# Optimization experiments

Hardware: AMD Instinct MI355X
Metric: run time of the kernel (lower is better)

Reference implementation:

```python
import jax, jax.numpy as jnp
import numpy as np

B, S, D = 1, 2048, 2048
H, HKV = 16, 4
HD = D // H  # 128
E, TOPK, F = 8, 2, 2048
CLIP = 8.0
THETA = 500000.0
EPS = 1e-5


def setup_inputs() -> dict:
    key = jax.random.key(0)
    ks = jax.random.split(key, 12)
    s = lambda k, shape, scale: jax.random.normal(k, shape, dtype=jnp.float32) * scale
    return {
        "hidden_states": s(ks[0], (B, S, D), 1.0),
        "position_ids": jnp.broadcast_to(jnp.arange(S, dtype=jnp.int32), (B, S)),
        "ln1_w": jnp.ones((D,), jnp.float32),
        "ln1_b": jnp.zeros((D,), jnp.float32),
        "ln2_w": jnp.ones((D,), jnp.float32),
        "ln2_b": jnp.zeros((D,), jnp.float32),
        "Wqkv": s(ks[1], (D, (H + 2 * HKV) * HD), 0.02),
        "Wout": s(ks[2], (D, D), 0.02),
        "Wrouter": s(ks[3], (D, E), 0.02),
        "w1": s(ks[4], (E, D, F), 0.02),
        "v1": s(ks[5], (E, D, F), 0.02),
        "w2": s(ks[6], (E, F, D), 0.02),
    }


def _layernorm(x, w, b):
    mu = jnp.mean(x, axis=-1, keepdims=True)
    var = jnp.mean((x - mu) ** 2, axis=-1, keepdims=True)
    return (x - mu) * jax.lax.rsqrt(var + EPS) * w + b


def _rope(x, pos):
    # x: [B,S,h,HD], neox style (rotate halves)
    half = HD // 2
    inv_freq = 1.0 / (THETA ** (jnp.arange(0, HD, 2, dtype=jnp.float32) / HD))
    ang = pos.astype(jnp.float32)[..., None] * inv_freq  # [B,S,half]
    cos = jnp.cos(ang)[:, :, None, :]
    sin = jnp.sin(ang)[:, :, None, :]
    x1, x2 = x[..., :half], x[..., half:]
    return jnp.concatenate([x1 * cos - x2 * sin, x2 * cos + x1 * sin], axis=-1)


def _forward(hidden_states, position_ids, ln1_w, ln1_b, ln2_w, ln2_b,
             Wqkv, Wout, Wrouter, w1, v1, w2):
    residual = hidden_states
    h = _layernorm(hidden_states, ln1_w, ln1_b)
    qkv = jnp.clip(h @ Wqkv, -CLIP, CLIP)
    q, k, v = jnp.split(qkv, [H * HD, H * HD + HKV * HD], axis=-1)
    q = q.reshape(B, S, H, HD)
    k = k.reshape(B, S, HKV, HD)
    v = v.reshape(B, S, HKV, HD)
    q = _rope(q, position_ids)
    k = _rope(k, position_ids)
    # GQA: repeat kv heads
    rep = H // HKV
    k = jnp.repeat(k, rep, axis=2)
    v = jnp.repeat(v, rep, axis=2)
    scale = HD ** -0.5
    scores = jnp.einsum("bqhd,bkhd->bhqk", q, k) * scale
    causal = jnp.tril(jnp.ones((S, S), dtype=bool))
    scores = jnp.where(causal, scores, jnp.float32(-1e9))
    probs = jax.nn.softmax(scores, axis=-1)
    attn = jnp.einsum("bhqk,bkhd->bqhd", probs, v).reshape(B, S, D)
    attn = attn @ Wout
    h = residual + attn
    residual = h
    h = _layernorm(h, ln2_w, ln2_b)

    # MoE over flattened tokens
    x = h.reshape(-1, D)  # [T,D]
    logits = x @ Wrouter  # [T,E]
    rw = jax.nn.softmax(logits.astype(jnp.float32), axis=-1)
    top_w, top_idx = jax.lax.top_k(rw, TOPK)  # [T,TOPK]
    top_w = top_w / jnp.sum(top_w, axis=-1, keepdims=True)
    acc = jnp.zeros_like(x)
    for e in range(E):  # fixed small expert count, matches source structure
        ew = jnp.sum(top_w * (top_idx == e), axis=-1, keepdims=True)  # [T,1]
        inter = jax.nn.silu(x @ w1[e]) * (x @ v1[e])
        acc = acc + (inter @ w2[e]) * ew
    out = acc.reshape(B, S, D) + residual
    return out


def reference(hidden_states, position_ids, ln1_w, ln1_b, ln2_w, ln2_b,
              Wqkv, Wout, Wrouter, w1, v1, w2):
    return _forward(hidden_states, position_ids, ln1_w, ln1_b, ln2_w, ln2_b,
                    Wqkv, Wout, Wrouter, w1, v1, w2)
```

## Files before the change

kernel.cpp:

```cpp
#include <hip/hip_runtime.h>
#include <cstdint>
#include <cstddef>
#include <cmath>

typedef unsigned short u16;
typedef unsigned int u32;
typedef __attribute__((ext_vector_type(8))) _Float16 f16x8;
typedef __attribute__((ext_vector_type(4))) float f32x4;

#define S_LEN 2048
#define DMODEL 2048
#define NHEAD 16
#define NKVH 4
#define HDIM 128
#define NQKV 3072
#define NF 2048
#define TA 4096
#define ATT_SCALE 0.08838834764831845f
#define LO_SCALE 1024.0f
#define LO_INV (1.0f/1024.0f)
#define DEFER_THR 8.0f

static __device__ __forceinline__ u16 f2h(float x){ _Float16 h=(_Float16)x; return __builtin_bit_cast(u16,h); }
static __device__ __forceinline__ float h2f(u16 u){ return (float)__builtin_bit_cast(_Float16,u); }
static __device__ __forceinline__ void split2(float x, u16& hi, u16& lo){
  hi = f2h(x);
  lo = f2h((x - h2f(hi)) * LO_SCALE);
}
static __device__ __forceinline__ void gload16(const u16* g, u16* l){
  __builtin_amdgcn_global_load_lds(
      (const __attribute__((address_space(1))) void*)g,
      (__attribute__((address_space(3))) void*)l, 16, 0, 0);
}
static __device__ __forceinline__ void xcd_swz(int& bx, int& by){
  int gx = gridDim.x;
  int n = gx * gridDim.y;
  int bid = by*gx + bx;
  int cpx = n >> 3;
  int s = (bid & 7)*cpx + (bid >> 3);
  bx = s % gx; by = s / gx;
}

#define WS_WOUTH ((size_t)0)
#define WS_WOUTL ((size_t)8388608)
#define WS_QKVTH ((size_t)16777216)
#define WS_QKVTL ((size_t)29360128)
#define WS_H1H   ((size_t)41943040)
#define WS_H1L   ((size_t)50331648)
#define WS_QKV   ((size_t)58720256)
#define WS_QH    ((size_t)16777216)
#define WS_QL    ((size_t)25165824)
#define WS_KH    ((size_t)33554432)
#define WS_KL    ((size_t)35651584)
#define WS_VTH   ((size_t)37748736)
#define WS_VTL   ((size_t)39845888)
#define WS_OH    ((size_t)41943040)
#define WS_OL    ((size_t)50331648)
#define WS_H2    ((size_t)58720256)
#define WS_X2    ((size_t)75497472)
#define WS_I1    ((size_t)0)
#define WS_Y     ((size_t)16777216)
#define WS_MOE   ((size_t)33554432)
#define WS_SM    ((size_t)83886080)
#define WS_WT0   ((size_t)84934656)
#define WS_WT1   ((size_t)152043520)
#define WS_BIG   ((size_t)219152384)
#define SM_INVT   0
#define SM_COUNTS 256
#define SM_FILL   320
#define SM_OFFS   384
#define SM_NT     448
#define SM_TE     512
#define SM_TRS    768
#define SM_E01    1024
#define SM_W01    (1024+16384)
#define SM_ATOK   (1024+2*16384)
#define SM_AW     (1024+3*16384)
#define SM_SLOT   (1024+4*16384)

__global__ void __launch_bounds__(64) init_k(int* counts, int* fill, float* invt){
  int t = threadIdx.x;
  if (t < 8) { counts[t] = 0; fill[t] = 0; }
  double di = (double)t * (1.0/64.0);
  float y = (float)pow(500000.0, di);
  invt[t] = 1.0f / y;
}

__global__ void __launch_bounds__(256) wsplit_k(const float* __restrict__ W,
    u16* __restrict__ Th, u16* __restrict__ Tl, int N){
  __shared__ float tile[32][33];
  int n0 = blockIdx.x*32, k0 = blockIdx.y*32;
  int tid = threadIdx.x;
  int rr = tid >> 3, cg = tid & 7;
  #pragma unroll
  for (int j=0;j<4;++j)
    tile[rr][cg*4+j] = W[(size_t)(k0+rr)*N + n0 + cg*4 + j];
  __syncthreads();
  int cc = tid >> 3, sg = tid & 7;
  #pragma unroll
  for (int j=0;j<4;++j){
    float x = tile[sg*4+j][cc];
    u16 hi, lo; split2(x, hi, lo);
    size_t idx = (size_t)(n0+cc)*2048 + k0 + sg*4 + j;
    Th[idx] = hi; Tl[idx] = lo;
  }
}

__global__ void __launch_bounds__(256) wconvT_k(const float* __restrict__ W,
                                                u16* __restrict__ T){
  __shared__ float tile[64][68];
  int n0 = blockIdx.x*64, k0 = blockIdx.y*64;
  size_t ebase = (size_t)blockIdx.z * 2048 * 2048;
  int tid = threadIdx.x;
  int rr = tid >> 4, c4 = (tid & 15)*4;
  #pragma unroll
  for (int p=0;p<4;++p){
    float4 v = *(const float4*)(W + ebase + (size_t)(k0+p*16+rr)*2048 + n0 + c4);
    *(float4*)&tile[p*16+rr][c4] = v;
  }
  __syncthreads();
  int nn = tid >> 2, kc = (tid & 3)*16;
  u16 buf[16];
  #pragma unroll
  for (int j=0;j<16;++j) buf[j] = f2h(tile[kc+j][nn]);
  u16* dst = T + ebase + (size_t)(n0+nn)*2048 + k0 + kc;
  *(int4*)dst = *(int4*)&buf[0];
  *(int4*)(dst+8) = *(int4*)&buf[8];
}

__device__ __forceinline__ float blk_red_sum(float v, float* red, int tid){
  #pragma unroll
  for (int off=1; off<64; off<<=1) v += __shfl_xor(v, off);
  if ((tid&63)==0) red[tid>>6] = v;
  __syncthreads();
  float r = red[0]+red[1]+red[2]+red[3];
  __syncthreads();
  return r;
}

__global__ void __launch_bounds__(256) ln1_k(const float* __restrict__ X,
    const float* __restrict__ W, const float* __restrict__ Bv,
    u16* __restrict__ Hh, u16* __restrict__ Hl){
  __shared__ float red[4];
  int t = blockIdx.x, tid = threadIdx.x;
  const float* row = X + (size_t)t*DMODEL + tid*8;
  float4 a = *(const float4*)row;
  float4 b = *(const float4*)(row+4);
  float xs[8] = {a.x,a.y,a.z,a.w,b.x,b.y,b.z,b.w};
  float s = 0.f;
  #pragma unroll
  for (int j=0;j<8;++j) s += xs[j];
  float mu = blk_red_sum(s, red, tid) * (1.f/DMODEL);
  float sq = 0.f;
  #pragma unroll
  for (int j=0;j<8;++j){ float d = xs[j]-mu; sq += d*d; }
  float var = blk_red_sum(sq, red, tid) * (1.f/DMODEL);
  float rs = 1.0f/sqrtf(var + 1e-5f);
  float4 w0 = *(const float4*)(W + tid*8);
  float4 w1 = *(const float4*)(W + tid*8 + 4);
  float4 b0 = *(const float4*)(Bv + tid*8);
  float4 b1 = *(const float4*)(Bv + tid*8 + 4);
  float ws_[8] = {w0.x,w0.y,w0.z,w0.w,w1.x,w1.y,w1.z,w1.w};
  float bs_[8] = {b0.x,b0.y,b0.z,b0.w,b1.x,b1.y,b1.z,b1.w};
  u32 ph[4], pl[4];
  #pragma unroll
  for (int j=0;j<4;++j){
    u16 h0,l0,h1,l1;
    split2((xs[2*j]-mu)*rs*ws_[2*j]+bs_[2*j], h0, l0);
    split2((xs[2*j+1]-mu)*rs*ws_[2*j+1]+bs_[2*j+1], h1, l1);
    ph[j] = (u32)h0 | ((u32)h1<<16);
    pl[j] = (u32)l0 | ((u32)l1<<16);
  }
  int4 vh; vh.x=(int)ph[0]; vh.y=(int)ph[1]; vh.z=(int)ph[2]; vh.w=(int)ph[3];
  int4 vl; vl.x=(int)pl[0]; vl.y=(int)pl[1]; vl.z=(int)pl[2]; vl.w=(int)pl[3];
  *(int4*)(Hh + (size_t)t*DMODEL + tid*8) = vh;
  *(int4*)(Hl + (size_t)t*DMODEL + tid*8) = vl;
}

template<int MODE>
__global__ void __launch_bounds__(256) gemm32_k(
    const u16* __restrict__ Ahp, const u16* __restrict__ Alp,
    const u16* __restrict__ Bhp, const u16* __restrict__ Blp,
    float* __restrict__ C, const float* __restrict__ res)
{
  constexpr int K = 2048;
  __shared__ u16 Ash[128*32], Asl[128*32], Bsh[64*32], Bsl[64*32];
  int bx = blockIdx.x, by = blockIdx.y;
  xcd_swz(bx, by);
  int m0 = by*128, n0 = bx*64;
  int tid = threadIdx.x, w = tid>>6, lane = tid&63;
  int l15 = lane&15, l4 = lane>>4, wr = w>>1, wc = w&1;
  int srow = lane>>2;
  int scol = ((lane&3) ^ ((lane>>3)&3))*8;

  f32x4 accH[4][2] = {}, accC[4][2] = {};

  for (int k0 = 0; k0 < K; k0 += 32){
    __syncthreads();
    #pragma unroll
    for (int c=0;c<2;++c){
      int row = w*32 + c*16 + srow;
      size_t ga = (size_t)(m0+row)*K + k0 + scol;
      gload16(Ahp+ga, &Ash[(w*32+c*16)*32]);
      gload16(Alp+ga, &Asl[(w*32+c*16)*32]);
    }
    {
      int rowb = w*16 + srow;
      size_t gb = (size_t)(n0+rowb)*K + k0 + scol;
      gload16(Bhp+gb, &Bsh[(w*16)*32]);
      gload16(Blp+gb, &Bsl[(w*16)*32]);
    }
    __syncthreads();
    int fsl = (l4 ^ ((l15>>1)&3))*8;
    f16x8 ah[4], al[4];
    #pragma unroll
    for (int mi=0; mi<4; ++mi){
      int row = wr*64 + mi*16 + l15;
      ah[mi] = *(const f16x8*)&Ash[row*32 + fsl];
      al[mi] = *(const f16x8*)&Asl[row*32 + fsl];
    }
    #pragma unroll
    for (int ni=0; ni<2; ++ni){
      int row = wc*32 + ni*16 + l15;
      f16x8 bh = *(const f16x8*)&Bsh[row*32 + fsl];
      f16x8 bl = *(const f16x8*)&Bsl[row*32 + fsl];
      #pragma unroll
      for (int mi=0; mi<4; ++mi){
        accH[mi][ni] = __builtin_amdgcn_mfma_f32_16x16x32_f16(ah[mi], bh, accH[mi][ni], 0,0,0);
        accC[mi][ni] = __builtin_amdgcn_mfma_f32_16x16x32_f16(ah[mi], bl, accC[mi][ni], 0,0,0);
        accC[mi][ni] = __builtin_amdgcn_mfma_f32_16x16x32_f16(al[mi], bh, accC[mi][ni], 0,0,0);
      }
    }
  }

  #pragma unroll
  for (int mi=0; mi<4; ++mi){
    #pragma unroll
    for (int ni=0; ni<2; ++ni){
      #pragma unroll
      for (int r=0; r<4; ++r){
        int rl = wr*64 + mi*16 + l4*4 + r;
        int cl = wc*32 + ni*16 + l15;
        float v = accH[mi][ni][r] + accC[mi][ni][r]*LO_INV;
        if constexpr (MODE == 0){
          v = fminf(fmaxf(v, -8.f), 8.f);
          C[(size_t)(m0 + rl)*NQKV + n0 + cl] = v;
        } else {
          size_t idx = (size_t)(m0 + rl)*DMODEL + n0 + cl;
          C[idx] = v + res[idx];
        }
      }
    }
  }
}

__global__ void __launch_bounds__(256) rope_k(const float* __restrict__ qkv,
    const int* __restrict__ pos_ids, const float* __restrict__ invt,
    u16* __restrict__ Qh, u16* __restrict__ Ql, u16* __restrict__ Kh, u16* __restrict__ Kl){
  int s = blockIdx.x;
  float pos = (float)pos_ids[s];
  const float* row = qkv + (size_t)s*NQKV;
  for (int p = threadIdx.x; p < 1280; p += 256){
    int i = p & 63;
    float ang = pos * invt[i];
    float sn, cs;
    sincosf(ang, &sn, &cs);
    u16 h1_,l1_,h2_,l2_;
    if (p < 1024){
      int h = p >> 6;
      float x1 = row[h*HDIM + i];
      float x2 = row[h*HDIM + 64 + i];
      size_t base = ((size_t)h*S_LEN + s)*HDIM;
      split2(x1*cs - x2*sn, h1_, l1_);
      split2(x2*cs + x1*sn, h2_, l2_);
      Qh[base + i] = h1_; Ql[base + i] = l1_;
      Qh[base + 64 + i] = h2_; Ql[base + 64 + i] = l2_;
    } else {
      int kh = (p-1024) >> 6;
      float x1 = row[2048 + kh*HDIM + i];
      float x2 = row[2048 + kh*HDIM + 64 + i];
      size_t base = ((size_t)kh*S_LEN + s)*HDIM;
      split2(x1*cs - x2*sn, h1_, l1_);
      split2(x2*cs + x1*sn, h2_, l2_);
      Kh[base + i] = h1_; Kl[base + i] = l1_;
      Kh[base + 64 + i] = h2_; Kl[base + 64 + i] = l2_;
    }
  }
}

__global__ void __launch_bounds__(256) vtrans_k(const float* __restrict__ qkv,
    u16* __restrict__ Vth, u16* __restrict__ Vtl){
  __shared__ float tile[32][33];
  int s0 = blockIdx.x*32, c0 = blockIdx.y*32;
  int tid = threadIdx.x;
  int rr = tid >> 3, cg = tid & 7;
  #pragma unroll
  for (int j=0;j<4;++j)
    tile[rr][cg*4+j] = qkv[(size_t)(s0+rr)*NQKV + 2560 + c0 + cg*4 + j];
  __syncthreads();
  int cc = tid >> 3, sg = tid & 7;
  #pragma unroll
  for (int j=0;j<4;++j){
    float x = tile[sg*4+j][cc];
    u16 hi, lo; split2(x, hi, lo);
    size_t idx = (size_t)(c0+cc)*S_LEN + s0 + sg*4 + j;
    Vth[idx] = hi; Vtl[idx] = lo;
  }
}

__global__ void __launch_bounds__(256) attn_k(
    const u16* __restrict__ Qhp, const u16* __restrict__ Qlp,
    const u16* __restrict__ Khp, const u16* __restrict__ Klp,
    const u16* __restrict__ Vthp, const u16* __restrict__ Vtlp,
    u16* __restrict__ Oh, u16* __restrict__ Ol){
  __shared__ u16 Ksh[32*128], Ksl[32*128];
  __shared__ u16 Vsh[128*32], Vsl[128*32];
  __shared__ u16 Psh[4*16*40], Psl[4*16*40];
  int tid = threadIdx.x;
  int w = tid>>6, lane = tid&63, l15 = lane&15, l4 = lane>>4;
  int qb = 31 - blockIdx.x;
  int h = blockIdx.y, kvh = h>>2;
  int q0 = qb*64 + w*16;
  f16x8 qfh[4], qfl[4];
  #pragma unroll
  for (int ds=0; ds<4; ++ds){
    size_t off = ((size_t)h*S_LEN + q0 + l15)*HDIM + ds*32 + l4*8;
    qfh[ds] = *(const f16x8*)(Qhp + off);
    qfl[ds] = *(const f16x8*)(Qlp + off);
  }
  f32x4 accH[8] = {}, accC[8] = {};
  float m_r[4], l_r[4];
  #pragma unroll
  for (int r=0;r<4;++r){ m_r[r] = -1e30f; l_r[r] = 0.f; }
  int ntile = 2*qb + 2;
  for (int kb = 0; kb < ntile; ++kb){
    int kbase = kb*32;
    __syncthreads();
    #pragma unroll
    for (int c=0;c<2;++c){
      int krow = w*8 + c*4 + (lane>>4);
      int ks = lane&15;
      int kcol = ((ks&8) | ((ks&7) ^ (krow&7)))*8;
      size_t koff = ((size_t)kvh*S_LEN + kbase + krow)*HDIM + kcol;
      gload16(Khp + koff, &Ksh[(w*8+c*4)*128]);
      gload16(Klp + koff, &Ksl[(w*8+c*4)*128]);
      int vrow = w*32 + c*16 + (lane>>2);
      int vcol = (((lane&3) ^ ((lane>>3)&3)))*8;
      size_t voff = ((size_t)kvh*HDIM + vrow)*S_LEN + kbase + vcol;
      gload16(Vthp + voff, &Vsh[(w*32+c*16)*32]);
      gload16(Vtlp + voff, &Vsl[(w*32+c*16)*32]);
    }
    __syncthreads();
    f32x4 sH0 = {}, sH1 = {}, sC0 = {}, sC1 = {};
    #pragma unroll
    for (int ds=0; ds<4; ++ds){
      int ksl = ds*4 + l4;
      int klds = ((ksl&8) | ((ksl&7) ^ (l15&7)))*8;
      f16x8 kh0 = *(const f16x8*)&Ksh[l15*128 + klds];
      f16x8 kl0 = *(const f16x8*)&Ksl[l15*128 + klds];
      f16x8 kh1 = *(const f16x8*)&Ksh[(16+l15)*128 + klds];
      f16x8 kl1 = *(const f16x8*)&Ksl[(16+l15)*128 + klds];
      sH0 = __builtin_amdgcn_mfma_f32_16x16x32_f16(qfh[ds], kh0, sH0, 0,0,0);
      sC0 = __builtin_amdgcn_mfma_f32_16x16x32_f16(qfh[ds], kl0, sC0, 0,0,0);
      sC0 = __builtin_amdgcn_mfma_f32_16x16x32_f16(qfl[ds], kh0, sC0, 0,0,0);
      sH1 = __builtin_amdgcn_mfma_f32_16x16x32_f16(qfh[ds], kh1, sH1, 0,0,0);
      sC1 = __builtin_amdgcn_mfma_f32_16x16x32_f16(qfh[ds], kl1, sC1, 0,0,0);
      sC1 = __builtin_amdgcn_mfma_f32_16x16x32_f16(qfl[ds], kh1, sC1, 0,0,0);
    }
    float v0[4], v1[4];
    bool need = false;
    #pragma unroll
    for (int r=0;r<4;++r){
      int qg = q0 + l4*4 + r;
      v0[r] = (sH0[r] + sC0[r]*LO_INV)*ATT_SCALE; if (kbase + l15 > qg) v0[r] = -1e9f;
      v1[r] = (sH1[r] + sC1[r]*LO_INV)*ATT_SCALE; if (kbase + 16 + l15 > qg) v1[r] = -1e9f;
      float pm = fmaxf(v0[r], v1[r]);
      need = need || (pm > m_r[r] + DEFER_THR);
    }
    if (__any(need)){
      float fac[4];
      #pragma unroll
      for (int r=0;r<4;++r){
        float mx = fmaxf(v0[r], v1[r]);
        mx = fmaxf(mx, __shfl_xor(mx,1));
        mx = fmaxf(mx, __shfl_xor(mx,2));
        mx = fmaxf(mx, __shfl_xor(mx,4));
        mx = fmaxf(mx, __shfl_xor(mx,8));
        float mnew = fmaxf(m_r[r], mx);
        fac[r] = __expf(m_r[r] - mnew);
        l_r[r] *= fac[r];
        m_r[r] = mnew;
      }
      #pragma unroll
      for (int nt=0; nt<8; ++nt){
        #pragma unroll
        for (int r=0;r<4;++r){ accH[nt][r] *= fac[r]; accC[nt][r] *= fac[r]; }
      }
    }
    #pragma unroll
    for (int r=0;r<4;++r){
      float p0 = __expf(v0[r] - m_r[r]);
      float p1 = __expf(v1[r] - m_r[r]);
      l_r[r] += p0 + p1;
      u16 hi, lo;
      split2(p0, hi, lo);
      Psh[w*640 + (l4*4+r)*40 + l15] = hi;
      Psl[w*640 + (l4*4+r)*40 + l15] = lo;
      split2(p1, hi, lo);
      Psh[w*640 + (l4*4+r)*40 + 16 + l15] = hi;
      Psl[w*640 + (l4*4+r)*40 + 16 + l15] = lo;
    }
    f16x8 pfh = *(const f16x8*)&Psh[w*640 + l15*40 + l4*8];
    f16x8 pfl = *(const f16x8*)&Psl[w*640 + l15*40 + l4*8];
    #pragma unroll
    for (int nt=0; nt<8; ++nt){
      int vsl = (l4 ^ ((l15>>1)&3))*8;
      f16x8 vh = *(const f16x8*)&Vsh[(nt*16 + l15)*32 + vsl];
      f16x8 vl = *(const f16x8*)&Vsl[(nt*16 + l15)*32 + vsl];
      accH[nt] = __builtin_amdgcn_mfma_f32_16x16x32_f16(pfh, vh, accH[nt], 0,0,0);
      f32x4 aC = __builtin_amdgcn_mfma_f32_16x16x32_f16(pfh, vl, accC[nt], 0,0,0);
      accC[nt] = __builtin_amdgcn_mfma_f32_16x16x32_f16(pfl, vh, aC, 0,0,0);
    }
  }
  #pragma unroll
  for (int r=0;r<4;++r){
    float l = l_r[r];
    l += __shfl_xor(l,1); l += __shfl_xor(l,2);
    l += __shfl_xor(l,4); l += __shfl_xor(l,8);
    l_r[r] = l;
  }
  #pragma unroll
  for (int nt=0; nt<8; ++nt){
    #pragma unroll
    for (int r=0;r<4;++r){
      int row = q0 + l4*4 + r;
      int col = h*HDIM + nt*16 + l15;
      float val = (accH[nt][r] + accC[nt][r]*LO_INV) / l_r[r];
      u16 hi, lo; split2(val, hi, lo);
      Oh[(size_t)row*DMODEL + col] = hi;
      Ol[(size_t)row*DMODEL + col] = lo;
    }
  }
}

__global__ void __launch_bounds__(256) ln2_router_k(const float* __restrict__ H2,
    const float* __restrict__ W, const float* __restrict__ Bv,
    const float* __restrict__ Wr, u16* __restrict__ X2,
    int* __restrict__ e01, float* __restrict__ w01, int* __restrict__ counts){
  __shared__ float red[4];
  __shared__ float lred[4][8];
  int t = blockIdx.x, tid = threadIdx.x;
  const float* row = H2 + (size_t)t*DMODEL + tid*8;
  float4 a = *(const float4*)row;
  float4 b = *(const float4*)(row+4);
  float xs[8] = {a.x,a.y,a.z,a.w,b.x,b.y,b.z,b.w};
  float s = 0.f;
  #pragma unroll
  for (int j=0;j<8;++j) s += xs[j];
  float mu = blk_red_sum(s, red, tid) * (1.f/DMODEL);
  float sq = 0.f;
  #pragma unroll
  for (int j=0;j<8;++j){ float d = xs[j]-mu; sq += d*d; }
  float var = blk_red_sum(sq, red, tid) * (1.f/DMODEL);
  float rs = 1.0f/sqrtf(var + 1e-5f);
  float4 w0 = *(const float4*)(W + tid*8);
  float4 w1 = *(const float4*)(W + tid*8 + 4);
  float4 b0 = *(const float4*)(Bv + tid*8);
  float4 b1 = *(const float4*)(Bv + tid*8 + 4);
  float ws_[8] = {w0.x,w0.y,w0.z,w0.w,w1.x,w1.y,w1.z,w1.w};
  float bs_[8] = {b0.x,b0.y,b0.z,b0.w,b1.x,b1.y,b1.z,b1.w};
  float xn[8];
  #pragma unroll
  for (int j=0;j<8;++j) xn[j] = (xs[j]-mu)*rs*ws_[j]+bs_[j];
  u32 pk[4];
  #pragma unroll
  for (int j=0;j<4;++j) pk[j] = (u32)f2h(xn[2*j]) | ((u32)f2h(xn[2*j+1])<<16);
  int4 v; v.x=(int)pk[0]; v.y=(int)pk[1]; v.z=(int)pk[2]; v.w=(int)pk[3];
  *(int4*)(X2 + (size_t)t*DMODEL + tid*8) = v;
  float lg[8] = {0,0,0,0,0,0,0,0};
  #pragma unroll
  for (int j=0;j<8;++j){
    const float* wrp = Wr + (size_t)(tid*8 + j)*8;
    float4 wa = *(const float4*)wrp;
    float4 wb = *(const float4*)(wrp+4);
    lg[0]+=xn[j]*wa.x; lg[1]+=xn[j]*wa.y; lg[2]+=xn[j]*wa.z; lg[3]+=xn[j]*wa.w;
    lg[4]+=xn[j]*wb.x; lg[5]+=xn[j]*wb.y; lg[6]+=xn[j]*wb.z; lg[7]+=xn[j]*wb.w;
  }
  #pragma unroll
  for (int e=0;e<8;++e){
    #pragma unroll
    for (int off=1; off<64; off<<=1) lg[e] += __shfl_xor(lg[e], off);
  }
  if ((tid&63)==0){
    #pragma unroll
    for (int e=0;e<8;++e) lred[tid>>6][e] = lg[e];
  }
  __syncthreads();
  if (tid==0){
    float L[8];
    #pragma unroll
    for (int e=0;e<8;++e) L[e] = lred[0][e]+lred[1][e]+lred[2][e]+lred[3][e];
    int e0 = 0;
    #pragma unroll
    for (int e=1;e<8;++e) if (L[e] > L[e0]) e0 = e;
    int e1 = (e0==0)?1:0;
    #pragma unroll
    for (int e=0;e<8;++e) if (e!=e0 && L[e] > L[e1]) e1 = e;
    float ax = expf(L[e1]-L[e0]);
    float z = 1.f/(1.f+ax);
    e01[2*t] = e0; e01[2*t+1] = e1;
    w01[2*t] = z;  w01[2*t+1] = ax*z;
    atomicAdd(&counts[e0],1); atomicAdd(&counts[e1],1);
  }
}

__global__ void __launch_bounds__(64) htiles_k(const int* counts, int* offs, int* ntl,
                                               int* te, int* trs){
  if (threadIdx.x==0){
    int off=0;
    for (int e=0;e<8;++e){ offs[e]=off; off+=counts[e]; }
    offs[8]=off;
    int nt=0;
    for (int e=0;e<8;++e)
      for (int j=0; j*128 < counts[e]; ++j){ te[nt]=e; trs[nt]=j*128; nt++; }
    ntl[0]=nt;
  }
}

__global__ void __launch_bounds__(256) scatter_k(const int* __restrict__ e01,
    const float* __restrict__ w01, const int* __restrict__ offs, int* __restrict__ fill,
    int* __restrict__ atok, float* __restrict__ aw, int* __restrict__ slots){
  int t = blockIdx.x*256 + threadIdx.x;
  if (t >= S_LEN) return;
  int e0 = e01[2*t], e1 = e01[2*t+1];
  int p0 = offs[e0] + atomicAdd(&fill[e0],1);
  atok[p0] = t; aw[p0] = w01[2*t]; slots[2*t] = p0;
  int p1 = offs[e1] + atomicAdd(&fill[e1],1);
  atok[p1] = t; aw[p1] = w01[2*t+1]; slots[2*t+1] = p1;
}

__global__ void __launch_bounds__(256) gemm_moe13_k(
    const u16* __restrict__ A, const u16* __restrict__ B1T, const u16* __restrict__ B2T,
    u16* __restrict__ Y,
    const int* __restrict__ atok, const int* __restrict__ counts,
    const int* __restrict__ offs, const int* __restrict__ ntl,
    const int* __restrict__ te, const int* __restrict__ trs)
{
  constexpr int K = 2048;
  __shared__ u16 As[128*32], B1s[64*32], B2s[64*32];
  int bx = blockIdx.x, by = blockIdx.y;
  xcd_swz(bx, by);
  if (by >= ntl[0]) return;
  int e = te[by];
  int rsu = trs[by];
  int base = offs[e] + rsu;
  int valid = min(128, counts[e] - rsu);
  const u16* B1p = B1T + (size_t)e * 2048 * 2048;
  const u16* B2p = B2T + (size_t)e * 2048 * 2048;
  int tid = threadIdx.x, w = tid>>6, lane = tid&63;
  int l15 = lane & 15, l4 = lane >> 4;
  int wr = w >> 1, wc = w & 1;
  int srow = lane>>2;
  int scol = ((lane&3) ^ ((lane>>3)&3))*8;
  int n0 = bx*64;
  int tokc[2];
  #pragma unroll
  for (int c=0;c<2;++c){
    int rr = w*32 + c*16 + srow;
    tokc[c] = atok[min(base + rr, TA-1)] & (S_LEN-1);
  }

  f32x4 acc1[4][2] = {}, acc2[4][2] = {};

  for (int k0 = 0; k0 < K; k0 += 32){
    __syncthreads();
    #pragma unroll
    for (int c=0;c<2;++c)
      gload16(A + (size_t)tokc[c]*K + k0 + scol, &As[(w*32+c*16)*32]);
    {
      int rowb = w*16 + srow;
      size_t gb = (size_t)(n0+rowb)*K + k0 + scol;
      gload16(B1p + gb, &B1s[(w*16)*32]);
      gload16(B2p + gb, &B2s[(w*16)*32]);
    }
    __syncthreads();
    int fsl = (l4 ^ ((l15>>1)&3))*8;
    f16x8 af[4];
    #pragma unroll
    for (int mi=0; mi<4; ++mi)
      af[mi] = *(const f16x8*)&As[(wr*64 + mi*16 + l15)*32 + fsl];
    #pragma unroll
    for (int ni=0; ni<2; ++ni){
      int row = wc*32 + ni*16 + l15;
      f16x8 b1 = *(const f16x8*)&B1s[row*32 + fsl];
      f16x8 b2 = *(const f16x8*)&B2s[row*32 + fsl];
      #pragma unroll
      for (int mi=0; mi<4; ++mi){
        acc1[mi][ni] = __builtin_amdgcn_mfma_f32_16x16x32_f16(af[mi], b1, acc1[mi][ni], 0,0,0);
        acc2[mi][ni] = __builtin_amdgcn_mfma_f32_16x16x32_f16(af[mi], b2, acc2[mi][ni], 0,0,0);
      }
    }
  }

  #pragma unroll
  for (int mi=0; mi<4; ++mi){
    #pragma unroll
    for (int ni=0; ni<2; ++ni){
      #pragma unroll
      for (int r=0; r<4; ++r){
        int rl = wr*64 + mi*16 + l4*4 + r;
        if (rl >= valid) continue;
        int col = n0 + wc*32 + ni*16 + l15;
        float a = acc1[mi][ni][r];
        float sl = a / (1.f + __expf(-a));
        Y[(size_t)(base + rl)*NF + col] = f2h(sl * acc2[mi][ni][r]);
      }
    }
  }
}

template<int MODE>
__global__ void __launch_bounds__(256) gemm_moe_k(
    const u16* __restrict__ A, const u16* __restrict__ BT, void* __restrict__ C,
    const u16* __restrict__ i1g, const float* __restrict__ aw,
    const int* __restrict__ atok, const int* __restrict__ counts,
    const int* __restrict__ offs, const int* __restrict__ ntl,
    const int* __restrict__ te, const int* __restrict__ trs)
{
  constexpr int K = 2048;
  __shared__ u16 As[128*32], Bs[64*32];
  int bx = blockIdx.x, by = blockIdx.y;
  xcd_swz(bx, by);
  if (by >= ntl[0]) return;
  int e = te[by];
  int rsu = trs[by];
  int base = offs[e] + rsu;
  int valid = min(128, counts[e] - rsu);
  const u16* Bp = BT + (size_t)e * 2048 * 2048;
  int tid = threadIdx.x, w = tid>>6, lane = tid&63;
  int l15 = lane & 15, l4 = lane >> 4;
  int wr = w >> 1, wc = w & 1;
  int srow = lane>>2;
  int scol = ((lane&3) ^ ((lane>>3)&3))*8;
  int n0 = bx*64;
  int tokc[2];
  #pragma unroll
  for (int c=0;c<2;++c){
    int rr = w*32 + c*16 + srow;
    if constexpr (MODE == 2 || MODE == 3)
      tokc[c] = atok[min(base + rr, TA-1)] & (S_LEN-1);
    else
      tokc[c] = min(base + rr, TA-1);
  }

  f32x4 acc[4][2] = {};

  for (int k0 = 0; k0 < K; k0 += 32){
    __syncthreads();
    #pragma unroll
    for (int c=0;c<2;++c)
      gload16(A + (size_t)tokc[c]*K + k0 + scol, &As[(w*32+c*16)*32]);
    {
      int rowb = w*16 + srow;
      gload16(Bp + (size_t)(n0+rowb)*K + k0 + scol, &Bs[(w*16)*32]);
    }
    __syncthreads();
    int fsl = (l4 ^ ((l15>>1)&3))*8;
    f16x8 af[4];
    #pragma unroll
    for (int mi=0; mi<4; ++mi)
      af[mi] = *(const f16x8*)&As[(wr*64 + mi*16 + l15)*32 + fsl];
    #pragma unroll
    for (int ni=0; ni<2; ++ni){
      f16x8 bfv = *(const f16x8*)&Bs[(wc*32 + ni*16 + l15)*32 + fsl];
      #pragma unroll
      for (int mi=0; mi<4; ++mi)
        acc[mi][ni] = __builtin_amdgcn_mfma_f32_16x16x32_f16(af[mi], bfv, acc[mi][ni], 0,0,0);
    }
  }

  #pragma unroll
  for (int mi=0; mi<4; ++mi){
    #pragma unroll
    for (int ni=0; ni<2; ++ni){
      f32x4 v = acc[mi][ni];
      #pragma unroll
      for (int r=0; r<4; ++r){
        int rl = wr*64 + mi*16 + l4*4 + r;
        if (rl >= valid) continue;
        int col = n0 + wc*32 + ni*16 + l15;
        if constexpr (MODE == 2){
          ((u16*)C)[(size_t)(base + rl)*NF + col] = f2h(v[r]);
        } else if constexpr (MODE == 3){
          size_t idx = (size_t)(base + rl)*NF + col;
          float a = h2f(i1g[idx]);
          float sl = a / (1.f + __expf(-a));
          ((u16*)C)[idx] = f2h(sl * v[r]);
        } else {
          float wgt = aw[base + rl];
          ((u16*)C)[(size_t)(base + rl)*DMODEL + col] = f2h(v[r] * wgt);
        }
      }
    }
  }
}

__global__ void __launch_bounds__(256) combine_k(const float* __restrict__ H2,
    const u16* __restrict__ MOE, const int* __restrict__ slots, float* __restrict__ out){
  int t = blockIdx.x, tid = threadIdx.x;
  int s0 = slots[2*t], s1 = slots[2*t+1];
  const float* h2p = H2 + (size_t)t*DMODEL + tid*8;
  int4 b0 = *(const int4*)(MOE + (size_t)s0*DMODEL + tid*8);
  int4 b1 = *(const int4*)(MOE + (size_t)s1*DMODEL + tid*8);
  const u16* bp0 = (const u16*)&b0;
  const u16* bp1 = (const u16*)&b1;
  float* op = out + (size_t)t*DMODEL + tid*8;
  #pragma unroll
  for (int j=0;j<8;++j)
    op[j] = h2p[j] + h2f(bp0[j]) + h2f(bp1[j]);
}

extern "C" void kernel_launch(void* const* d_in, const int* in_sizes, int n_in,
                              void* d_out, int out_size, void* d_ws, size_t ws_size,
                              hipStream_t stream){
  const float* hidden = (const float*)d_in[0];
  const int*   pos    = (const int*)d_in[1];
  const float* ln1w   = (const float*)d_in[2];
  const float* ln1b   = (const float*)d_in[3];
  const float* ln2w   = (const float*)d_in[4];
  const float* ln2b   = (const float*)d_in[5];
  const float* Wqkv   = (const float*)d_in[6];
  const float* Wout   = (const float*)d_in[7];
  const float* Wr     = (const float*)d_in[8];
  const float* w1     = (const float*)d_in[9];
  const float* v1     = (const float*)d_in[10];
  const float* w2     = (const float*)d_in[11];
  float* out = (float*)d_out;
  char* ws = (char*)d_ws;

  u16* woutTh = (u16*)(ws + WS_WOUTH);
  u16* woutTl = (u16*)(ws + WS_WOUTL);
  u16* qkvTh  = (u16*)(ws + WS_QKVTH);
  u16* qkvTl  = (u16*)(ws + WS_QKVTL);
  u16* h1h = (u16*)(ws + WS_H1H);
  u16* h1l = (u16*)(ws + WS_H1L);
  float* qkv = (float*)(ws + WS_QKV);
  u16* Qh = (u16*)(ws + WS_QH);
  u16* Ql = (u16*)(ws + WS_QL);
  u16* Kh = (u16*)(ws + WS_KH);
  u16* Kl = (u16*)(ws + WS_KL);
  u16* Vth = (u16*)(ws + WS_VTH);
  u16* Vtl = (u16*)(ws + WS_VTL);
  u16* Oh = (u16*)(ws + WS_OH);
  u16* Ol = (u16*)(ws + WS_OL);
  float* h2 = (float*)(ws + WS_H2);
  u16* x2 = (u16*)(ws + WS_X2);
  u16* i1 = (u16*)(ws + WS_I1);
  u16* Yb = (u16*)(ws + WS_Y);
  u16* moe = (u16*)(ws + WS_MOE);
  u16* wT0 = (u16*)(ws + WS_WT0);
  u16* wT1 = (u16*)(ws + WS_WT1);
  char* sm = ws + WS_SM;
  float* invt = (float*)(sm + SM_INVT);
  int* counts = (int*)(sm + SM_COUNTS);
  int* fill   = (int*)(sm + SM_FILL);
  int* offs   = (int*)(sm + SM_OFFS);
  int* ntl    = (int*)(sm + SM_NT);
  int* te     = (int*)(sm + SM_TE);
  int* trs    = (int*)(sm + SM_TRS);
  int* e01    = (int*)(sm + SM_E01);
  float* w01  = (float*)(sm + SM_W01);
  int* atok   = (int*)(sm + SM_ATOK);
  float* aw   = (float*)(sm + SM_AW);
  int* slots  = (int*)(sm + SM_SLOT);

  init_k<<<1, 64, 0, stream>>>(counts, fill, invt);
  wsplit_k<<<dim3(96,64), 256, 0, stream>>>(Wqkv, qkvTh, qkvTl, NQKV);
  wsplit_k<<<dim3(64,64), 256, 0, stream>>>(Wout, woutTh, woutTl, DMODEL);
  ln1_k<<<S_LEN, 256, 0, stream>>>(hidden, ln1w, ln1b, h1h, h1l);
  gemm32_k<0><<<dim3(48,16), 256, 0, stream>>>(h1h, h1l, qkvTh, qkvTl, qkv, nullptr);
  rope_k<<<S_LEN, 256, 0, stream>>>(qkv, pos, invt, Qh, Ql, Kh, Kl);
  vtrans_k<<<dim3(64,16), 256, 0, stream>>>(qkv, Vth, Vtl);
  attn_k<<<dim3(32,16), 256, 0, stream>>>(Qh, Ql, Kh, Kl, Vth, Vtl, Oh, Ol);
  gemm32_k<1><<<dim3(32,16), 256, 0, stream>>>(Oh, Ol, woutTh, woutTl, h2, hidden);
  ln2_router_k<<<S_LEN, 256, 0, stream>>>(h2, ln2w, ln2b, Wr, x2, e01, w01, counts);
  htiles_k<<<1, 64, 0, stream>>>(counts, offs, ntl, te, trs);
  scatter_k<<<8, 256, 0, stream>>>(e01, w01, offs, fill, atok, aw, slots);
  if (ws_size >= WS_BIG){
    wconvT_k<<<dim3(32,32,8), 256, 0, stream>>>(w1, wT0);
    wconvT_k<<<dim3(32,32,8), 256, 0, stream>>>(v1, wT1);
    gemm_moe13_k<<<dim3(32,40), 256, 0, stream>>>(x2, wT0, wT1, Yb,
        atok, counts, offs, ntl, te, trs);
    wconvT_k<<<dim3(32,32,8), 256, 0, stream>>>(w2, wT0);
    gemm_moe_k<4><<<dim3(32,40), 256, 0, stream>>>(Yb, wT0, moe, nullptr, aw,
        atok, counts, offs, ntl, te, trs);
  } else {
    wconvT_k<<<dim3(32,32,8), 256, 0, stream>>>(w1, wT0);
    gemm_moe_k<2><<<dim3(32,40), 256, 0, stream>>>(x2, wT0, i1, nullptr, nullptr,
        atok, counts, offs, ntl, te, trs);
    wconvT_k<<<dim3(32,32,8), 256, 0, stream>>>(v1, wT0);
    gemm_moe_k<3><<<dim3(32,40), 256, 0, stream>>>(x2, wT0, Yb, i1, nullptr,
        atok, counts, offs, ntl, te, trs);
    wconvT_k<<<dim3(32,32,8), 256, 0, stream>>>(w2, wT0);
    gemm_moe_k<4><<<dim3(32,40), 256, 0, stream>>>(Yb, wT0, moe, nullptr, aw,
        atok, counts, offs, ntl, te, trs);
  }
  combine_k<<<S_LEN, 256, 0, stream>>>(h2, moe, slots, out);
}
```

Baseline: 791.5 us.

## Double-buffer LDS tiles in GEMM and attention kernels, tweak attention scheduling

Gives the split-precision QKV/out GEMM, both MoE GEMMs and the attention kernel two LDS buffers each. The next K tile (or KV tile) is now prefetched while the current one is consumed, which removes one barrier per iteration and overlaps global-to-LDS loads with MFMA work. Attention also raises wave priority around its MFMA blocks and applies the causal mask only on diagonal tiles. It alternates the query-block order between head halves to balance the causal workload. The cost is doubled shared-memory use per block, which may lower occupancy, most of all in attention.

```diff
diff --git a/kernel.cpp b/kernel.cpp
--- a/kernel.cpp
+++ b/kernel.cpp
@@ -184,7 +184,7 @@
     float* __restrict__ C, const float* __restrict__ res)
 {
   constexpr int K = 2048;
-  __shared__ u16 Ash[128*32], Asl[128*32], Bsh[64*32], Bsl[64*32];
+  __shared__ u16 Ash[2][128*32], Asl[2][128*32], Bsh[2][64*32], Bsl[2][64*32];
   int bx = blockIdx.x, by = blockIdx.y;
   xcd_swz(bx, by);
   int m0 = by*128, n0 = bx*64;
@@ -195,35 +195,38 @@
 
   f32x4 accH[4][2] = {}, accC[4][2] = {};
 
-  for (int k0 = 0; k0 < K; k0 += 32){
-    __syncthreads();
+  auto stage = [&](int k0, int b){
     #pragma unroll
     for (int c=0;c<2;++c){
       int row = w*32 + c*16 + srow;
       size_t ga = (size_t)(m0+row)*K + k0 + scol;
-      gload16(Ahp+ga, &Ash[(w*32+c*16)*32]);
-      gload16(Alp+ga, &Asl[(w*32+c*16)*32]);
-    }
-    {
-      int rowb = w*16 + srow;
-      size_t gb = (size_t)(n0+rowb)*K + k0 + scol;
-      gload16(Bhp+gb, &Bsh[(w*16)*32]);
-      gload16(Blp+gb, &Bsl[(w*16)*32]);
-    }
+      gload16(Ahp+ga, &Ash[b][(w*32+c*16)*32]);
+      gload16(Alp+ga, &Asl[b][(w*32+c*16)*32]);
+    }
+    int rowb = w*16 + srow;
+    size_t gb = (size_t)(n0+rowb)*K + k0 + scol;
+    gload16(Bhp+gb, &Bsh[b][(w*16)*32]);
+    gload16(Blp+gb, &Bsl[b][(w*16)*32]);
+  };
+
+  stage(0, 0);
+  int cur = 0;
+  for (int k0 = 0; k0 < K; k0 += 32){
     __syncthreads();
+    if (k0 + 32 < K) stage(k0 + 32, cur^1);
     int fsl = (l4 ^ ((l15>>1)&3))*8;
     f16x8 ah[4], al[4];
     #pragma unroll
     for (int mi=0; mi<4; ++mi){
       int row = wr*64 + mi*16 + l15;
-      ah[mi] = *(const f16x8*)&Ash[row*32 + fsl];
-      al[mi] = *(const f16x8*)&Asl[row*32 + fsl];
+      ah[mi] = *(const f16x8*)&Ash[cur][row*32 + fsl];
+      al[mi] = *(const f16x8*)&Asl[cur][row*32 + fsl];
     }
     #pragma unroll
     for (int ni=0; ni<2; ++ni){
       int row = wc*32 + ni*16 + l15;
-      f16x8 bh = *(const f16x8*)&Bsh[row*32 + fsl];
-      f16x8 bl = *(const f16x8*)&Bsl[row*32 + fsl];
+      f16x8 bh = *(const f16x8*)&Bsh[cur][row*32 + fsl];
+      f16x8 bl = *(const f16x8*)&Bsl[cur][row*32 + fsl];
       #pragma unroll
       for (int mi=0; mi<4; ++mi){
         accH[mi][ni] = __builtin_amdgcn_mfma_f32_16x16x32_f16(ah[mi], bh, accH[mi][ni], 0,0,0);
@@ -231,6 +234,7 @@
         accC[mi][ni] = __builtin_amdgcn_mfma_f32_16x16x32_f16(al[mi], bh, accC[mi][ni], 0,0,0);
       }
     }
+    cur ^= 1;
   }
 
   #pragma unroll
@@ -313,13 +317,13 @@
     const u16* __restrict__ Khp, const u16* __restrict__ Klp,
     const u16* __restrict__ Vthp, const u16* __restrict__ Vtlp,
     u16* __restrict__ Oh, u16* __restrict__ Ol){
-  __shared__ u16 Ksh[32*128], Ksl[32*128];
-  __shared__ u16 Vsh[128*32], Vsl[128*32];
+  __shared__ u16 Ksh[2][32*128], Ksl[2][32*128];
+  __shared__ u16 Vsh[2][128*32], Vsl[2][128*32];
   __shared__ u16 Psh[4*16*40], Psl[4*16*40];
   int tid = threadIdx.x;
   int w = tid>>6, lane = tid&63, l15 = lane&15, l4 = lane>>4;
-  int qb = 31 - blockIdx.x;
   int h = blockIdx.y, kvh = h>>2;
+  int qb = (h < 8) ? (31 - blockIdx.x) : blockIdx.x;
   int q0 = qb*64 + w*16;
   f16x8 qfh[4], qfl[4];
   #pragma unroll
@@ -333,33 +337,41 @@
   #pragma unroll
   for (int r=0;r<4;++r){ m_r[r] = -1e30f; l_r[r] = 0.f; }
   int ntile = 2*qb + 2;
+
+  auto stageKV = [&](int kb, int b){
+    int kbase = kb*32;
+    #pragma unroll
+    for (int c=0;c<2;++c){
+      int krow = w*8 + c*4 + l4;
+      int ks = l15;
+      int kcol = ((ks&8) | ((ks&7) ^ (krow&7)))*8;
+      size_t koff = ((size_t)kvh*S_LEN + kbase + krow)*HDIM + kcol;
+      gload16(Khp + koff, &Ksh[b][(w*8+c*4)*128]);
+      gload16(Klp + koff, &Ksl[b][(w*8+c*4)*128]);
+      int vrow = w*32 + c*16 + (lane>>2);
+      int vcol = ((lane&3) ^ ((lane>>3)&3))*8;
+      size_t voff = ((size_t)kvh*HDIM + vrow)*S_LEN + kbase + vcol;
+      gload16(Vthp + voff, &Vsh[b][(w*32+c*16)*32]);
+      gload16(Vtlp + voff, &Vsl[b][(w*32+c*16)*32]);
+    }
+  };
+
+  stageKV(0, 0);
+  int cur = 0;
   for (int kb = 0; kb < ntile; ++kb){
     int kbase = kb*32;
     __syncthreads();
-    #pragma unroll
-    for (int c=0;c<2;++c){
-      int krow = w*8 + c*4 + (lane>>4);
-      int ks = lane&15;
-      int kcol = ((ks&8) | ((ks&7) ^ (krow&7)))*8;
-      size_t koff = ((size_t)kvh*S_LEN + kbase + krow)*HDIM + kcol;
-      gload16(Khp + koff, &Ksh[(w*8+c*4)*128]);
-      gload16(Klp + koff, &Ksl[(w*8+c*4)*128]);
-      int vrow = w*32 + c*16 + (lane>>2);
-      int vcol = (((lane&3) ^ ((lane>>3)&3)))*8;
-      size_t voff = ((size_t)kvh*HDIM + vrow)*S_LEN + kbase + vcol;
-      gload16(Vthp + voff, &Vsh[(w*32+c*16)*32]);
-      gload16(Vtlp + voff, &Vsl[(w*32+c*16)*32]);
-    }
-    __syncthreads();
+    if (kb + 1 < ntile) stageKV(kb + 1, cur^1);
     f32x4 sH0 = {}, sH1 = {}, sC0 = {}, sC1 = {};
+    __builtin_amdgcn_s_setprio(1);
     #pragma unroll
     for (int ds=0; ds<4; ++ds){
       int ksl = ds*4 + l4;
       int klds = ((ksl&8) | ((ksl&7) ^ (l15&7)))*8;
-      f16x8 kh0 = *(const f16x8*)&Ksh[l15*128 + klds];
-      f16x8 kl0 = *(const f16x8*)&Ksl[l15*128 + klds];
-      f16x8 kh1 = *(const f16x8*)&Ksh[(16+l15)*128 + klds];
-      f16x8 kl1 = *(const f16x8*)&Ksl[(16+l15)*128 + klds];
+      f16x8 kh0 = *(const f16x8*)&Ksh[cur][l15*128 + klds];
+      f16x8 kl0 = *(const f16x8*)&Ksl[cur][l15*128 + klds];
+      f16x8 kh1 = *(const f16x8*)&Ksh[cur][(16+l15)*128 + klds];
+      f16x8 kl1 = *(const f16x8*)&Ksl[cur][(16+l15)*128 + klds];
       sH0 = __builtin_amdgcn_mfma_f32_16x16x32_f16(qfh[ds], kh0, sH0, 0,0,0);
       sC0 = __builtin_amdgcn_mfma_f32_16x16x32_f16(qfh[ds], kl0, sC0, 0,0,0);
       sC0 = __builtin_amdgcn_mfma_f32_16x16x32_f16(qfl[ds], kh0, sC0, 0,0,0);
@@ -367,13 +379,19 @@
       sC1 = __builtin_amdgcn_mfma_f32_16x16x32_f16(qfh[ds], kl1, sC1, 0,0,0);
       sC1 = __builtin_amdgcn_mfma_f32_16x16x32_f16(qfl[ds], kh1, sC1, 0,0,0);
     }
+    __builtin_amdgcn_s_setprio(0);
     float v0[4], v1[4];
+    bool diag = (kbase + 31 > q0);
     bool need = false;
     #pragma unroll
     for (int r=0;r<4;++r){
-      int qg = q0 + l4*4 + r;
-      v0[r] = (sH0[r] + sC0[r]*LO_INV)*ATT_SCALE; if (kbase + l15 > qg) v0[r] = -1e9f;
-      v1[r] = (sH1[r] + sC1[r]*LO_INV)*ATT_SCALE; if (kbase + 16 + l15 > qg) v1[r] = -1e9f;
+      v0[r] = (sH0[r] + sC0[r]*LO_INV)*ATT_SCALE;
+      v1[r] = (sH1[r] + sC1[r]*LO_INV)*ATT_SCALE;
+      if (diag){
+        int qg = q0 + l4*4 + r;
+        if (kbase + l15 > qg) v0[r] = -1e9f;
+        if (kbase + 16 + l15 > qg) v1[r] = -1e9f;
+      }
       float pm = fmaxf(v0[r], v1[r]);
       need = need || (pm > m_r[r] + DEFER_THR);
     }
@@ -412,15 +430,18 @@
     }
     f16x8 pfh = *(const f16x8*)&Psh[w*640 + l15*40 + l4*8];
     f16x8 pfl = *(const f16x8*)&Psl[w*640 + l15*40 + l4*8];
+    __builtin_amdgcn_s_setprio(1);
     #pragma unroll
     for (int nt=0; nt<8; ++nt){
       int vsl = (l4 ^ ((l15>>1)&3))*8;
-      f16x8 vh = *(const f16x8*)&Vsh[(nt*16 + l15)*32 + vsl];
-      f16x8 vl = *(const f16x8*)&Vsl[(nt*16 + l15)*32 + vsl];
+      f16x8 vh = *(const f16x8*)&Vsh[cur][(nt*16 + l15)*32 + vsl];
+      f16x8 vl = *(const f16x8*)&Vsl[cur][(nt*16 + l15)*32 + vsl];
       accH[nt] = __builtin_amdgcn_mfma_f32_16x16x32_f16(pfh, vh, accH[nt], 0,0,0);
       f32x4 aC = __builtin_amdgcn_mfma_f32_16x16x32_f16(pfh, vl, accC[nt], 0,0,0);
       accC[nt] = __builtin_amdgcn_mfma_f32_16x16x32_f16(pfl, vh, aC, 0,0,0);
     }
+    __builtin_amdgcn_s_setprio(0);
+    cur ^= 1;
   }
   #pragma unroll
   for (int r=0;r<4;++r){
@@ -547,7 +568,7 @@
     const int* __restrict__ te, const int* __restrict__ trs)
 {
   constexpr int K = 2048;
-  __shared__ u16 As[128*32], B1s[64*32], B2s[64*32];
+  __shared__ u16 As[2][128*32], B1s[2][64*32], B2s[2][64*32];
   int bx = blockIdx.x, by = blockIdx.y;
   xcd_swz(bx, by);
   if (by >= ntl[0]) return;
@@ -572,34 +593,38 @@
 
   f32x4 acc1[4][2] = {}, acc2[4][2] = {};
 
+  auto stage = [&](int k0, int b){
+    #pragma unroll
+    for (int c=0;c<2;++c)
+      gload16(A + (size_t)tokc[c]*K + k0 + scol, &As[b][(w*32+c*16)*32]);
+    int rowb = w*16 + srow;
+    size_t gb = (size_t)(n0+rowb)*K + k0 + scol;
+    gload16(B1p + gb, &B1s[b][(w*16)*32]);
+    gload16(B2p + gb, &B2s[b][(w*16)*32]);
+  };
+
+  stage(0, 0);
+  int cur = 0;
   for (int k0 = 0; k0 < K; k0 += 32){
     __syncthreads();
-    #pragma unroll
-    for (int c=0;c<2;++c)
-      gload16(A + (size_t)tokc[c]*K + k0 + scol, &As[(w*32+c*16)*32]);
-    {
-      int rowb = w*16 + srow;
-      size_t gb = (size_t)(n0+rowb)*K + k0 + scol;
-      gload16(B1p + gb, &B1s[(w*16)*32]);
-      gload16(B2p + gb, &B2s[(w*16)*32]);
-    }
-    __syncthreads();
+    if (k0 + 32 < K) stage(k0 + 32, cur^1);
     int fsl = (l4 ^ ((l15>>1)&3))*8;
     f16x8 af[4];
     #pragma unroll
     for (int mi=0; mi<4; ++mi)
-      af[mi] = *(const f16x8*)&As[(wr*64 + mi*16 + l15)*32 + fsl];
+      af[mi] = *(const f16x8*)&As[cur][(wr*64 + mi*16 + l15)*32 + fsl];
     #pragma unroll
     for (int ni=0; ni<2; ++ni){
       int row = wc*32 + ni*16 + l15;
-      f16x8 b1 = *(const f16x8*)&B1s[row*32 + fsl];
-      f16x8 b2 = *(const f16x8*)&B2s[row*32 + fsl];
+      f16x8 b1 = *(const f16x8*)&B1s[cur][row*32 + fsl];
+      f16x8 b2 = *(const f16x8*)&B2s[cur][row*32 + fsl];
       #pragma unroll
       for (int mi=0; mi<4; ++mi){
         acc1[mi][ni] = __builtin_amdgcn_mfma_f32_16x16x32_f16(af[mi], b1, acc1[mi][ni], 0,0,0);
         acc2[mi][ni] = __builtin_amdgcn_mfma_f32_16x16x32_f16(af[mi], b2, acc2[mi][ni], 0,0,0);
       }
     }
+    cur ^= 1;
   }
 
   #pragma unroll
@@ -628,7 +653,7 @@
     const int* __restrict__ te, const int* __restrict__ trs)
 {
   constexpr int K = 2048;
-  __shared__ u16 As[128*32], Bs[64*32];
+  __shared__ u16 As[2][128*32], Bs[2][64*32];
   int bx = blockIdx.x, by = blockIdx.y;
   xcd_swz(bx, by);
   if (by >= ntl[0]) return;
@@ -655,28 +680,32 @@
 
   f32x4 acc[4][2] = {};
 
+  auto stage = [&](int k0, int b){
+    #pragma unroll
+    for (int c=0;c<2;++c)
+      gload16(A + (size_t)tokc[c]*K + k0 + scol, &As[b][(w*32+c*16)*32]);
+    int rowb = w*16 + srow;
+    gload16(Bp + (size_t)(n0+rowb)*K + k0 + scol, &Bs[b][(w*16)*32]);
+  };
+
+  stage(0, 0);
+  int cur = 0;
   for (int k0 = 0; k0 < K; k0 += 32){
     __syncthreads();
-    #pragma unroll
-    for (int c=0;c<2;++c)
-      gload16(A + (size_t)tokc[c]*K + k0 + scol, &As[(w*32+c*16)*32]);
-    {
-      int rowb = w*16 + srow;
-      gload16(Bp + (size_t)(n0+rowb)*K + k0 + scol, &Bs[(w*16)*32]);
-    }
-    __syncthreads();
+    if (k0 + 32 < K) stage(k0 + 32, cur^1);
     int fsl = (l4 ^ ((l15>>1)&3))*8;
     f16x8 af[4];
     #pragma unroll
     for (int mi=0; mi<4; ++mi)
-      af[mi] = *(const f16x8*)&As[(wr*64 + mi*16 + l15)*32 + fsl];
+      af[mi] = *(const f16x8*)&As[cur][(wr*64 + mi*16 + l15)*32 + fsl];
     #pragma unroll
     for (int ni=0; ni<2; ++ni){
-      f16x8 bfv = *(const f16x8*)&Bs[(wc*32 + ni*16 + l15)*32 + fsl];
+      f16x8 bfv = *(const f16x8*)&Bs[cur][(wc*32 + ni*16 + l15)*32 + fsl];
       #pragma unroll
       for (int mi=0; mi<4; ++mi)
         acc[mi][ni] = __builtin_amdgcn_mfma_f32_16x16x32_f16(af[mi], bfv, acc[mi][ni], 0,0,0);
     }
+    cur ^= 1;
   }
 
   #pragma unroll
```

Result: slower. 915.5 us (+15.7%).

## Split long causal attention rows across two blocks and merge partials

Applied to the files above, without the earlier changes.

Causal attention query blocks 16-31 now have their key range split in two, each half handled by a separate block. The halves write unnormalized partial outputs plus running max and sum, and a new merge kernel combines them. A longest-first schedule table built in init_k orders the 768 blocks to balance load, and launch bounds request 3 blocks per CU. The aim is to reduce tail imbalance across CUs, at the cost of an extra kernel launch and partial-result traffic through reused workspace buffers.

```diff
diff --git a/kernel.cpp b/kernel.cpp
--- a/kernel.cpp
+++ b/kernel.cpp
@@ -77,13 +77,42 @@
 #define SM_ATOK   (1024+2*16384)
 #define SM_AW     (1024+3*16384)
 #define SM_SLOT   (1024+4*16384)
-
-__global__ void __launch_bounds__(64) init_k(int* counts, int* fill, float* invt){
+#define SM_ITQ    82944
+#define SM_ITK0   83200
+#define SM_ITK1   83456
+#define SM_ITSL   83712
+
+__global__ void __launch_bounds__(64) init_k(int* counts, int* fill, float* invt,
+    int* itq, int* itk0, int* itk1, int* itsl){
   int t = threadIdx.x;
   if (t < 8) { counts[t] = 0; fill[t] = 0; }
   double di = (double)t * (1.0/64.0);
   float y = (float)pow(500000.0, di);
   invt[t] = 1.0f / y;
+  if (t == 0){
+    int qb_[48], k0_[48], k1_[48], sl_[48], sz_[48];
+    int n = 0;
+    for (int qb = 0; qb < 16; ++qb){
+      qb_[n]=qb; k0_[n]=0; k1_[n]=2*qb+2; sl_[n]=-1; sz_[n]=2*qb+2; n++;
+    }
+    for (int qb = 16; qb < 32; ++qb){
+      int half = qb + 1, nt = 2*qb + 2;
+      qb_[n]=qb; k0_[n]=0;    k1_[n]=half; sl_[n]=(qb-16)*2;   sz_[n]=half;    n++;
+      qb_[n]=qb; k0_[n]=half; k1_[n]=nt;   sl_[n]=(qb-16)*2+1; sz_[n]=nt-half; n++;
+    }
+    for (int i = 1; i < 48; ++i){
+      int q=qb_[i], a=k0_[i], b=k1_[i], s=sl_[i], z=sz_[i];
+      int j = i - 1;
+      while (j >= 0 && sz_[j] < z){
+        qb_[j+1]=qb_[j]; k0_[j+1]=k0_[j]; k1_[j+1]=k1_[j]; sl_[j+1]=sl_[j]; sz_[j+1]=sz_[j];
+        j--;
+      }
+      qb_[j+1]=q; k0_[j+1]=a; k1_[j+1]=b; sl_[j+1]=s; sz_[j+1]=z;
+    }
+    for (int i = 0; i < 48; ++i){
+      itq[i]=qb_[i]; itk0[i]=k0_[i]; itk1[i]=k1_[i]; itsl[i]=sl_[i];
+    }
+  }
 }
 
 __global__ void __launch_bounds__(256) wsplit_k(const float* __restrict__ W,
@@ -308,18 +337,21 @@
   }
 }
 
-__global__ void __launch_bounds__(256) attn_k(
+__global__ void __launch_bounds__(256, 3) attn_k(
     const u16* __restrict__ Qhp, const u16* __restrict__ Qlp,
     const u16* __restrict__ Khp, const u16* __restrict__ Klp,
     const u16* __restrict__ Vthp, const u16* __restrict__ Vtlp,
-    u16* __restrict__ Oh, u16* __restrict__ Ol){
+    u16* __restrict__ Oh, u16* __restrict__ Ol,
+    const int* __restrict__ itq, const int* __restrict__ itk0,
+    const int* __restrict__ itk1, const int* __restrict__ itsl,
+    float* __restrict__ Opart, float* __restrict__ Mlp){
   __shared__ u16 Ksh[32*128], Ksl[32*128];
   __shared__ u16 Vsh[128*32], Vsl[128*32];
   __shared__ u16 Psh[4*16*40], Psl[4*16*40];
   int tid = threadIdx.x;
   int w = tid>>6, lane = tid&63, l15 = lane&15, l4 = lane>>4;
-  int qb = 31 - blockIdx.x;
-  int h = blockIdx.y, kvh = h>>2;
+  int rank = blockIdx.x >> 4, h = blockIdx.x & 15, kvh = h >> 2;
+  int qb = itq[rank], kb0 = itk0[rank], kb1 = itk1[rank], sl = itsl[rank];
   int q0 = qb*64 + w*16;
   f16x8 qfh[4], qfl[4];
   #pragma unroll
@@ -332,20 +364,19 @@
   float m_r[4], l_r[4];
   #pragma unroll
   for (int r=0;r<4;++r){ m_r[r] = -1e30f; l_r[r] = 0.f; }
-  int ntile = 2*qb + 2;
-  for (int kb = 0; kb < ntile; ++kb){
+  for (int kb = kb0; kb < kb1; ++kb){
     int kbase = kb*32;
     __syncthreads();
     #pragma unroll
     for (int c=0;c<2;++c){
-      int krow = w*8 + c*4 + (lane>>4);
-      int ks = lane&15;
+      int krow = w*8 + c*4 + l4;
+      int ks = l15;
       int kcol = ((ks&8) | ((ks&7) ^ (krow&7)))*8;
       size_t koff = ((size_t)kvh*S_LEN + kbase + krow)*HDIM + kcol;
       gload16(Khp + koff, &Ksh[(w*8+c*4)*128]);
       gload16(Klp + koff, &Ksl[(w*8+c*4)*128]);
       int vrow = w*32 + c*16 + (lane>>2);
-      int vcol = (((lane&3) ^ ((lane>>3)&3)))*8;
+      int vcol = ((lane&3) ^ ((lane>>3)&3))*8;
       size_t voff = ((size_t)kvh*HDIM + vrow)*S_LEN + kbase + vcol;
       gload16(Vthp + voff, &Vsh[(w*32+c*16)*32]);
       gload16(Vtlp + voff, &Vsl[(w*32+c*16)*32]);
@@ -429,17 +460,67 @@
     l += __shfl_xor(l,4); l += __shfl_xor(l,8);
     l_r[r] = l;
   }
-  #pragma unroll
-  for (int nt=0; nt<8; ++nt){
-    #pragma unroll
-    for (int r=0;r<4;++r){
-      int row = q0 + l4*4 + r;
-      int col = h*HDIM + nt*16 + l15;
-      float val = (accH[nt][r] + accC[nt][r]*LO_INV) / l_r[r];
-      u16 hi, lo; split2(val, hi, lo);
-      Oh[(size_t)row*DMODEL + col] = hi;
-      Ol[(size_t)row*DMODEL + col] = lo;
-    }
+  if (sl < 0){
+    #pragma unroll
+    for (int nt=0; nt<8; ++nt){
+      #pragma unroll
+      for (int r=0;r<4;++r){
+        int row = q0 + l4*4 + r;
+        int col = h*HDIM + nt*16 + l15;
+        float val = (accH[nt][r] + accC[nt][r]*LO_INV) / l_r[r];
+        u16 hi, lo; split2(val, hi, lo);
+        Oh[(size_t)row*DMODEL + col] = hi;
+        Ol[(size_t)row*DMODEL + col] = lo;
+      }
+    }
+  } else {
+    int slot = sl*16 + h;
+    float* Op = Opart + (size_t)slot*8192;
+    #pragma unroll
+    for (int nt=0; nt<8; ++nt){
+      #pragma unroll
+      for (int r=0;r<4;++r){
+        int row = w*16 + l4*4 + r;
+        Op[row*128 + nt*16 + l15] = accH[nt][r] + accC[nt][r]*LO_INV;
+      }
+    }
+    if (l15 == 0){
+      #pragma unroll
+      for (int r=0;r<4;++r){
+        int row = w*16 + l4*4 + r;
+        Mlp[slot*128 + row*2]     = m_r[r];
+        Mlp[slot*128 + row*2 + 1] = l_r[r];
+      }
+    }
+  }
+}
+
+__global__ void __launch_bounds__(256) merge_k(const float* __restrict__ Op,
+    const float* __restrict__ Ml, u16* __restrict__ Oh, u16* __restrict__ Ol){
+  int qb = 16 + blockIdx.x, h = blockIdx.y;
+  int slot1 = ((qb-16)*2)*16 + h;
+  int slot2 = slot1 + 16;
+  int tid = threadIdx.x;
+  int rr = tid >> 2, cg = (tid & 3) * 32;
+  float m1 = Ml[slot1*128 + rr*2], l1 = Ml[slot1*128 + rr*2 + 1];
+  float m2 = Ml[slot2*128 + rr*2], l2 = Ml[slot2*128 + rr*2 + 1];
+  float M = fmaxf(m1, m2);
+  float a1 = __expf(m1 - M), a2 = __expf(m2 - M);
+  float inv = 1.f / (l1*a1 + l2*a2);
+  const float* p1 = Op + (size_t)slot1*8192 + rr*128 + cg;
+  const float* p2 = Op + (size_t)slot2*8192 + rr*128 + cg;
+  size_t ob = (size_t)(qb*64 + rr)*DMODEL + h*HDIM + cg;
+  #pragma unroll
+  for (int j = 0; j < 32; j += 4){
+    float4 o1 = *(const float4*)(p1 + j);
+    float4 o2 = *(const float4*)(p2 + j);
+    float vals[4] = {(o1.x*a1+o2.x*a2)*inv, (o1.y*a1+o2.y*a2)*inv,
+                     (o1.z*a1+o2.z*a2)*inv, (o1.w*a1+o2.w*a2)*inv};
+    u16 hs[4], ls[4];
+    #pragma unroll
+    for (int c=0;c<4;++c) split2(vals[c], hs[c], ls[c]);
+    *(uint2*)(Oh + ob + j) = *(uint2*)&hs[0];
+    *(uint2*)(Ol + ob + j) = *(uint2*)&ls[0];
   }
 }
 
@@ -760,6 +841,8 @@
   u16* moe = (u16*)(ws + WS_MOE);
   u16* wT0 = (u16*)(ws + WS_WT0);
   u16* wT1 = (u16*)(ws + WS_WT1);
+  float* Opart = (float*)(ws + WS_QKV);
+  float* Mlp   = (float*)(ws + WS_X2);
   char* sm = ws + WS_SM;
   float* invt = (float*)(sm + SM_INVT);
   int* counts = (int*)(sm + SM_COUNTS);
@@ -773,15 +856,21 @@
   int* atok   = (int*)(sm + SM_ATOK);
   float* aw   = (float*)(sm + SM_AW);
   int* slots  = (int*)(sm + SM_SLOT);
-
-  init_k<<<1, 64, 0, stream>>>(counts, fill, invt);
+  int* itq    = (int*)(sm + SM_ITQ);
+  int* itk0   = (int*)(sm + SM_ITK0);
+  int* itk1   = (int*)(sm + SM_ITK1);
+  int* itsl   = (int*)(sm + SM_ITSL);
+
+  init_k<<<1, 64, 0, stream>>>(counts, fill, invt, itq, itk0, itk1, itsl);
   wsplit_k<<<dim3(96,64), 256, 0, stream>>>(Wqkv, qkvTh, qkvTl, NQKV);
   wsplit_k<<<dim3(64,64), 256, 0, stream>>>(Wout, woutTh, woutTl, DMODEL);
   ln1_k<<<S_LEN, 256, 0, stream>>>(hidden, ln1w, ln1b, h1h, h1l);
   gemm32_k<0><<<dim3(48,16), 256, 0, stream>>>(h1h, h1l, qkvTh, qkvTl, qkv, nullptr);
   rope_k<<<S_LEN, 256, 0, stream>>>(qkv, pos, invt, Qh, Ql, Kh, Kl);
   vtrans_k<<<dim3(64,16), 256, 0, stream>>>(qkv, Vth, Vtl);
-  attn_k<<<dim3(32,16), 256, 0, stream>>>(Qh, Ql, Kh, Kl, Vth, Vtl, Oh, Ol);
+  attn_k<<<768, 256, 0, stream>>>(Qh, Ql, Kh, Kl, Vth, Vtl, Oh, Ol,
+      itq, itk0, itk1, itsl, Opart, Mlp);
+  merge_k<<<dim3(16,16), 256, 0, stream>>>(Opart, Mlp, Oh, Ol);
   gemm32_k<1><<<dim3(32,16), 256, 0, stream>>>(Oh, Ol, woutTh, woutTl, h2, hidden);
   ln2_router_k<<<S_LEN, 256, 0, stream>>>(h2, ln2w, ln2b, Wr, x2, e01, w01, counts);
   htiles_k<<<1, 64, 0, stream>>>(counts, offs, ntl, te, trs);
```

Measured after the change: 886.2 us. +12.0%, slower.
